# Optimization experiments

Measured on AMD Instinct MI355X. Metric: run time of the kernel, lower is better.

## Reference

```python
import jax, jax.numpy as jnp
import numpy as np

N, E = 50000, 800000
NFEAT, NHID, NCLASS = 128, 64, 40
NLAYERS = 4
DT, ALPHA, GAMMA = 1.0, 1.0, 1.0


def setup_inputs() -> dict:
    key = jax.random.key(0)
    ks = jax.random.split(key, 12)
    s = 1.0 / np.sqrt(NHID)
    inp = {
        'x': jax.random.normal(ks[0], (N, NFEAT), jnp.float32),
        'edge_index': jax.random.randint(ks[1], (2, E), 0, N, jnp.int64),
        # params stored as [in, out] matrices (torch Linear weight transposed)
        'enc_W': jax.random.uniform(ks[2], (NFEAT, NHID), jnp.float32, -s, s),
        'enc_b': jnp.zeros((NHID,), jnp.float32),
        'conv_W': jax.random.uniform(ks[3], (NHID, NHID), jnp.float32, -s, s),
        'conv_b': jnp.zeros((NHID,), jnp.float32),
        'res_W': jax.random.uniform(ks[4], (NHID, NHID), jnp.float32, -s, s),
        'res_b': jnp.zeros((NHID,), jnp.float32),
        'weight_mlp': jax.random.uniform(ks[5], (NHID, NHID), jnp.float32, -s, s),
        'lamda1': jnp.float32(1.0),
        'dec_W': jax.random.uniform(ks[6], (NHID, NCLASS), jnp.float32, -s, s),
        'dec_b': jnp.zeros((NCLASS,), jnp.float32),
    }
    return inp


def reference(x, edge_index, enc_W, enc_b, conv_W, conv_b, res_W, res_b,
              weight_mlp, lamda1, dec_W, dec_b):
    src, dst = edge_index[0], edge_index[1]
    # GCN symmetric normalization with self-loops (PyG GCNConv default)
    deg = jax.ops.segment_sum(jnp.ones((E,), x.dtype), dst, num_segments=N) + 1.0
    dinv = jax.lax.rsqrt(deg)                      # [N]
    enorm = (dinv[src] * dinv[dst])[:, None]       # [E,1]
    self_norm = (dinv * dinv)[:, None]             # [N,1]

    Y = jax.nn.relu(x @ enc_W + enc_b)             # [N,H]
    X = Y
    for _ in range(NLAYERS):
        Xs, Xd = X[src], X[dst]                    # [E,H] gathers
        x_new = jax.nn.relu((Xs - Xd) @ weight_mlp) * Xd
        ax3 = jax.ops.segment_sum(x_new, dst, num_segments=N)  # [N,H]
        # GCNConv: normalized aggregation of X@W plus self-loop, then bias
        xw = X @ conv_W
        conv = (jax.ops.segment_sum(xw[src] * enorm, dst, num_segments=N)
                + xw * self_norm + conv_b)
        # residual v1: -res(conv.lin(X)) = -(X@W_conv @ W_res + b_res)
        res = -(xw @ res_W + res_b)
        Y = Y + DT * (jax.nn.relu(conv + res) - ALPHA * Y - GAMMA * X)
        X = X + DT * (Y + lamda1 * ax3)
    return X @ dec_W + dec_b
```

## Files before the change

### kernel.cpp

```cpp
#include <hip/hip_runtime.h>

constexpr int H   = 64;
constexpr int NF  = 128;
constexpr int NC  = 40;
constexpr int CAP = 96;

typedef __attribute__((ext_vector_type(8))) short short8;
typedef __attribute__((ext_vector_type(4))) float f32x4;

constexpr int FRAG_ENC = 1536;
constexpr int FRAG_DEC = 3584;
constexpr int FRAG_TOT = 4352;

__device__ __forceinline__ unsigned int f2bf(float f) {
  unsigned int u = __float_as_uint(f);
  return (u + 0x7fffu + ((u >> 16) & 1u)) >> 16;
}
__device__ __forceinline__ float bf_lo(unsigned int v) { return __uint_as_float(v << 16); }
__device__ __forceinline__ float bf_hi(unsigned int v) { return __uint_as_float(v & 0xffff0000u); }
__device__ __forceinline__ short8 ld_frag(const uint4* frag, int idx) {
  uint4 u = frag[idx];
  short8 r; __builtin_memcpy(&r, &u, 16); return r;
}

__global__ void k_wcr(const float* __restrict__ Wconv, const float* __restrict__ resW,
                      float* __restrict__ Wcr) {
  int idx = blockIdx.x * 256 + threadIdx.x;
  int k = idx >> 6, n = idx & 63;
  float s = 0.0f;
  for (int j = 0; j < 64; ++j) s = fmaf(Wconv[k * 64 + j], resW[j * 64 + n], s);
  Wcr[idx] = s;
}

__global__ void k_prep(const float* __restrict__ Wmlp, const float* __restrict__ Wconv,
                       const float* __restrict__ Wcr, const float* __restrict__ encW,
                       const float* __restrict__ decW, uint4* __restrict__ frag) {
  int it = blockIdx.x * 256 + threadIdx.x;
  if (it >= FRAG_TOT) return;
  unsigned int h[8];
  if (it < FRAG_ENC) {
    int lane = it & 63;
    int kb = (it >> 6) & 1;
    int nb = (it >> 7) & 3;
    int w  = (it >> 9);
    int col = nb * 16 + (lane & 15);
    int k0 = kb * 32 + (lane >> 4) * 8;
    for (int i = 0; i < 8; ++i) {
      float v;
      if (w == 2)      v = Wcr[(k0 + i) * 64 + col];
      else if (w == 1) v = Wconv[(k0 + i) * 64 + col];
      else             v = Wmlp[(k0 + i) * 64 + col];
      h[i] = f2bf(v);
    }
  } else if (it < FRAG_DEC) {
    int e = it - FRAG_ENC;
    int lane = e & 63;
    int kb = (e >> 6) & 3;
    int nb = (e >> 8) & 3;
    int hh = (e >> 10);
    int col = nb * 16 + (lane & 15);
    int k0 = kb * 32 + (lane >> 4) * 8;
    for (int i = 0; i < 8; ++i) {
      float v = encW[(k0 + i) * H + col];
      unsigned int hb = f2bf(v);
      h[i] = (hh == 0) ? hb : f2bf(v - __uint_as_float(hb << 16));
    }
  } else {
    int e = it - FRAG_DEC;
    int lane = e & 63;
    int kb = (e >> 6) & 1;
    int hn = e >> 7;
    int nb = hn % 3, hh = hn / 3;
    int col = nb * 16 + (lane & 15);
    int k0 = kb * 32 + (lane >> 4) * 8;
    for (int i = 0; i < 8; ++i) {
      float v = (col < NC) ? decW[(k0 + i) * NC + col] : 0.0f;
      unsigned int hb = f2bf(v);
      h[i] = (hh == 0) ? hb : f2bf(v - __uint_as_float(hb << 16));
    }
  }
  uint4 u; u.x = h[0] | (h[1] << 16); u.y = h[2] | (h[3] << 16);
  u.z = h[4] | (h[5] << 16); u.w = h[6] | (h[7] << 16);
  frag[it] = u;
}

__global__ void __launch_bounds__(256)
k_buildenc(const float* __restrict__ x, const uint4* __restrict__ frag,
           const float* __restrict__ encb, float* __restrict__ X,
           const int* __restrict__ src, const int* __restrict__ dst,
           int* __restrict__ counts, unsigned short* __restrict__ srcs,
           int N, int E) {
  int nchunks = (E + 1023) >> 10;
  if ((int)blockIdx.x < nchunks) {
    int base = (blockIdx.x << 10) + threadIdx.x;
    int d[4], s[4], slot[4];
#pragma unroll
    for (int j = 0; j < 4; ++j) {
      int e = base + j * 256;
      bool v = e < E;
      d[j] = v ? dst[e] : -1;
      s[j] = v ? src[e] : 0;
    }
#pragma unroll
    for (int j = 0; j < 4; ++j)
      slot[j] = (d[j] >= 0) ? atomicAdd(&counts[d[j]], 1) : CAP;
#pragma unroll
    for (int j = 0; j < 4; ++j)
      if (d[j] >= 0 && slot[j] < CAP) srcs[d[j] * CAP + slot[j]] = (unsigned short)s[j];
  }
  int lane = threadIdx.x & 63;
  int row = lane & 15, g = lane >> 4;
  int wv = (blockIdx.x * blockDim.x + threadIdx.x) >> 6;
  int nwv = (gridDim.x * blockDim.x) >> 6;
  float bias[4];
#pragma unroll
  for (int nb = 0; nb < 4; ++nb) bias[nb] = encb[nb * 16 + row];
  int nrb = (N + 15) >> 4;
  for (int rb = wv; rb < nrb; rb += nwv) {
    int n0 = rb << 4;
    int rload = n0 + row; if (rload > N - 1) rload = N - 1;
    const float* xp = x + (size_t)rload * NF + g * 8;
    f32x4 acc[4];
#pragma unroll
    for (int nb = 0; nb < 4; ++nb) acc[nb] = (f32x4){bias[nb], bias[nb], bias[nb], bias[nb]};
#pragma unroll
    for (int kb = 0; kb < 4; ++kb) {
      float4 a0 = *(const float4*)(xp + kb * 32);
      float4 a1 = *(const float4*)(xp + kb * 32 + 4);
      float xv[8] = {a0.x, a0.y, a0.z, a0.w, a1.x, a1.y, a1.z, a1.w};
      short8 Ahi, Alo;
#pragma unroll
      for (int i = 0; i < 8; ++i) {
        unsigned int hb = f2bf(xv[i]);
        Ahi[i] = (short)hb;
        Alo[i] = (short)f2bf(xv[i] - __uint_as_float(hb << 16));
      }
#pragma unroll
      for (int nb = 0; nb < 4; ++nb) {
        short8 Bh = ld_frag(frag, FRAG_ENC + ((0 * 4 + nb) * 4 + kb) * 64 + lane);
        short8 Bl = ld_frag(frag, FRAG_ENC + ((1 * 4 + nb) * 4 + kb) * 64 + lane);
        acc[nb] = __builtin_amdgcn_mfma_f32_16x16x32_bf16(Ahi, Bh, acc[nb], 0, 0, 0);
        acc[nb] = __builtin_amdgcn_mfma_f32_16x16x32_bf16(Alo, Bh, acc[nb], 0, 0, 0);
        acc[nb] = __builtin_amdgcn_mfma_f32_16x16x32_bf16(Ahi, Bl, acc[nb], 0, 0, 0);
      }
    }
#pragma unroll
    for (int nb = 0; nb < 4; ++nb) {
      int col = nb * 16 + row;
#pragma unroll
      for (int j = 0; j < 4; ++j) {
        int n = n0 + g * 4 + j;
        if (n < N) X[(size_t)n * H + col] = fmaxf(acc[nb][j], 0.0f);
      }
    }
  }
}

__global__ void __launch_bounds__(256, 2)
k_xform(const float* __restrict__ X, const uint4* __restrict__ frag,
        const float* __restrict__ resb, const int* __restrict__ counts,
        unsigned int* __restrict__ xmwq, unsigned short* __restrict__ rbuf, int N) {
  int lane = threadIdx.x & 63;
  int row = lane & 15, g = lane >> 4;
  int wv = (blockIdx.x * blockDim.x + threadIdx.x) >> 6;
  int nwv = (gridDim.x * blockDim.x) >> 6;

  short8 B[3][4][2];
#pragma unroll
  for (int w = 0; w < 3; ++w)
#pragma unroll
    for (int nb = 0; nb < 4; ++nb)
#pragma unroll
      for (int kb = 0; kb < 2; ++kb)
        B[w][nb][kb] = ld_frag(frag, ((w * 4 + nb) * 2 + kb) * 64 + lane);
  float rbias[4];
#pragma unroll
  for (int nb = 0; nb < 4; ++nb) rbias[nb] = resb[nb * 16 + row];

  int nrb = (N + 15) >> 4;
  for (int rb = wv; rb < nrb; rb += nwv) {
    int n0 = rb << 4;
    int rload = n0 + row; if (rload > N - 1) rload = N - 1;
    const float* xp = X + (size_t)rload * H + g * 8;
    float xv[2][8];
    {
      float4 a0 = *(const float4*)(xp);
      float4 a1 = *(const float4*)(xp + 4);
      float4 b0 = *(const float4*)(xp + 32);
      float4 b1 = *(const float4*)(xp + 36);
      xv[0][0]=a0.x; xv[0][1]=a0.y; xv[0][2]=a0.z; xv[0][3]=a0.w;
      xv[0][4]=a1.x; xv[0][5]=a1.y; xv[0][6]=a1.z; xv[0][7]=a1.w;
      xv[1][0]=b0.x; xv[1][1]=b0.y; xv[1][2]=b0.z; xv[1][3]=b0.w;
      xv[1][4]=b1.x; xv[1][5]=b1.y; xv[1][6]=b1.z; xv[1][7]=b1.w;
    }
    short8 Ahi[2], Alo[2];
#pragma unroll
    for (int kb = 0; kb < 2; ++kb)
#pragma unroll
      for (int i = 0; i < 8; ++i) {
        float v = xv[kb][i];
        unsigned int hb = f2bf(v);
        Ahi[kb][i] = (short)hb;
        Alo[kb][i] = (short)f2bf(v - __uint_as_float(hb << 16));
      }
    f32x4 am[4], ac[4], ar[4];
#pragma unroll
    for (int nb = 0; nb < 4; ++nb) {
      am[nb] = (f32x4){0.f, 0.f, 0.f, 0.f};
      ac[nb] = (f32x4){0.f, 0.f, 0.f, 0.f};
      ar[nb] = (f32x4){rbias[nb], rbias[nb], rbias[nb], rbias[nb]};
    }
#pragma unroll
    for (int nb = 0; nb < 4; ++nb)
#pragma unroll
      for (int kb = 0; kb < 2; ++kb) {
        am[nb] = __builtin_amdgcn_mfma_f32_16x16x32_bf16(Ahi[kb], B[0][nb][kb], am[nb], 0, 0, 0);
        am[nb] = __builtin_amdgcn_mfma_f32_16x16x32_bf16(Alo[kb], B[0][nb][kb], am[nb], 0, 0, 0);
        ac[nb] = __builtin_amdgcn_mfma_f32_16x16x32_bf16(Ahi[kb], B[1][nb][kb], ac[nb], 0, 0, 0);
        ac[nb] = __builtin_amdgcn_mfma_f32_16x16x32_bf16(Alo[kb], B[1][nb][kb], ac[nb], 0, 0, 0);
        ar[nb] = __builtin_amdgcn_mfma_f32_16x16x32_bf16(Ahi[kb], B[2][nb][kb], ar[nb], 0, 0, 0);
        ar[nb] = __builtin_amdgcn_mfma_f32_16x16x32_bf16(Alo[kb], B[2][nb][kb], ar[nb], 0, 0, 0);
      }
    float dn4[4];
#pragma unroll
    for (int j = 0; j < 4; ++j) {
      int n = n0 + g * 4 + j; if (n > N - 1) n = N - 1;
      dn4[j] = rsqrtf((float)counts[n] + 1.0f);
    }
#pragma unroll
    for (int nb = 0; nb < 4; ++nb) {
      int col = nb * 16 + row;
#pragma unroll
      for (int j = 0; j < 4; ++j) {
        int n = n0 + g * 4 + j;
        if (n < N) {
          xmwq[(size_t)n * H + col] = f2bf(am[nb][j]) | (f2bf(ac[nb][j] * dn4[j]) << 16);
          rbuf[(size_t)n * H + col] = (unsigned short)f2bf(ar[nb][j]);
        }
      }
    }
  }
}

template<int DOX>
__global__ void __launch_bounds__(256)
k_updx(const unsigned int* __restrict__ xmwq_in, const unsigned short* __restrict__ rbuf_in,
       const unsigned short* __restrict__ srcs, const int* __restrict__ counts,
       const float* __restrict__ convb, const float* __restrict__ lam1,
       float* __restrict__ X, const uint4* __restrict__ frag,
       const float* __restrict__ resb,
       unsigned int* __restrict__ xmwq_out, unsigned short* __restrict__ rbuf_out, int N) {
  __shared__ float sX[16][68];
  int lane = threadIdx.x & 63;
  int w = threadIdx.x >> 6;
  int row = lane & 15, gg = lane >> 4;
  float cb = convb[lane];
  float lam = lam1[0];
  short8 Bw[3][2];
  float rbias = 0.0f;
  if (DOX) {
#pragma unroll
    for (int m = 0; m < 3; ++m)
#pragma unroll
      for (int kb = 0; kb < 2; ++kb)
        Bw[m][kb] = ld_frag(frag, ((m * 4 + w) * 2 + kb) * 64 + lane);
    rbias = resb[w * 16 + row];
  }
  int g = blockIdx.x;
  {
#pragma unroll
    for (int j = 0; j < 4; ++j) {
      int nig = w * 4 + j;
      int n = g * 16 + nig;
      bool act = n < N;
      int nn = act ? n : N - 1;
      size_t rowo = (size_t)nn * H + lane;
      unsigned int own = xmwq_in[rowo];
      float xmd = bf_lo(own), xwsd = bf_hi(own);
      float r = __uint_as_float((unsigned int)rbuf_in[rowo] << 16);
      float Xd = X[rowo];
      int cntfull = counts[nn];
      float dn = rsqrtf((float)cntfull + 1.0f);
      int cnt = cntfull < CAP ? cntfull : CAP;
      int sv0 = (lane < cnt) ? (int)srcs[nn * CAP + lane] : 0;
      int sv1 = (64 + lane < cnt) ? (int)srcs[nn * CAP + 64 + lane] : 0;
      float acc3 = 0.0f, accC = 0.0f;
      for (int e = 0; e < cnt; e += 16) {
        unsigned int v[16]; float m[16];
#pragma unroll
        for (int q = 0; q < 16; ++q) {
          int eq = e + q;
          bool valid = eq < cnt;
          int s = valid ? ((eq < 64) ? __builtin_amdgcn_readlane(sv0, eq)
                                     : __builtin_amdgcn_readlane(sv1, eq - 64))
                        : 0;
          v[q] = xmwq_in[(size_t)s * H + lane];
          m[q] = valid ? 1.0f : 0.0f;
        }
#pragma unroll
        for (int q = 0; q < 16; ++q) {
          acc3 += m[q] * fmaxf(bf_lo(v[q]) - xmd, 0.0f);
          accC += m[q] * bf_hi(v[q]);
        }
      }
      float conv = fmaf(dn, accC + xwsd, cb);
      float R = fmaxf(conv - r, 0.0f);
      float Xnew = R + lam * (acc3 * Xd);
      if (act) X[rowo] = Xnew;
      if (DOX) sX[nig][lane] = act ? Xnew : 0.0f;
    }
    if (DOX) {
      __syncthreads();
      short8 Ahi[2], Alo[2];
#pragma unroll
      for (int kb = 0; kb < 2; ++kb) {
        float4 a0 = *(const float4*)&sX[row][kb * 32 + gg * 8];
        float4 a1 = *(const float4*)&sX[row][kb * 32 + gg * 8 + 4];
        float xv[8] = {a0.x, a0.y, a0.z, a0.w, a1.x, a1.y, a1.z, a1.w};
#pragma unroll
        for (int i = 0; i < 8; ++i) {
          unsigned int hb = f2bf(xv[i]);
          Ahi[kb][i] = (short)hb;
          Alo[kb][i] = (short)f2bf(xv[i] - __uint_as_float(hb << 16));
        }
      }
      f32x4 am = (f32x4){0.f, 0.f, 0.f, 0.f};
      f32x4 ac = (f32x4){0.f, 0.f, 0.f, 0.f};
      f32x4 ar = (f32x4){rbias, rbias, rbias, rbias};
#pragma unroll
      for (int kb = 0; kb < 2; ++kb) {
        am = __builtin_amdgcn_mfma_f32_16x16x32_bf16(Ahi[kb], Bw[0][kb], am, 0, 0, 0);
        am = __builtin_amdgcn_mfma_f32_16x16x32_bf16(Alo[kb], Bw[0][kb], am, 0, 0, 0);
        ac = __builtin_amdgcn_mfma_f32_16x16x32_bf16(Ahi[kb], Bw[1][kb], ac, 0, 0, 0);
        ac = __builtin_amdgcn_mfma_f32_16x16x32_bf16(Alo[kb], Bw[1][kb], ac, 0, 0, 0);
        ar = __builtin_amdgcn_mfma_f32_16x16x32_bf16(Ahi[kb], Bw[2][kb], ar, 0, 0, 0);
        ar = __builtin_amdgcn_mfma_f32_16x16x32_bf16(Alo[kb], Bw[2][kb], ar, 0, 0, 0);
      }
      int col = w * 16 + row;
#pragma unroll
      for (int j = 0; j < 4; ++j) {
        int n = g * 16 + gg * 4 + j;
        if (n < N) {
          float dnn = rsqrtf((float)counts[n] + 1.0f);
          xmwq_out[(size_t)n * H + col] = f2bf(am[j]) | (f2bf(ac[j] * dnn) << 16);
          rbuf_out[(size_t)n * H + col] = (unsigned short)f2bf(ar[j]);
        }
      }
    }
  }
}

__global__ void __launch_bounds__(256)
k_dec(const float* __restrict__ X, const uint4* __restrict__ frag,
      const float* __restrict__ decb, float* __restrict__ out, int N) {
  int lane = threadIdx.x & 63;
  int row = lane & 15, g = lane >> 4;
  int wv = (blockIdx.x * blockDim.x + threadIdx.x) >> 6;
  int nwv = (gridDim.x * blockDim.x) >> 6;
  float bias[3];
#pragma unroll
  for (int nb = 0; nb < 3; ++nb) {
    int col = nb * 16 + row;
    bias[nb] = (col < NC) ? decb[col] : 0.0f;
  }
  int nrb = (N + 15) >> 4;
  for (int rb = wv; rb < nrb; rb += nwv) {
    int n0 = rb << 4;
    int rload = n0 + row; if (rload > N - 1) rload = N - 1;
    const float* xp = X + (size_t)rload * H + g * 8;
    f32x4 acc[3];
#pragma unroll
    for (int nb = 0; nb < 3; ++nb) acc[nb] = (f32x4){bias[nb], bias[nb], bias[nb], bias[nb]};
#pragma unroll
    for (int kb = 0; kb < 2; ++kb) {
      float4 a0 = *(const float4*)(xp + kb * 32);
      float4 a1 = *(const float4*)(xp + kb * 32 + 4);
      float xv[8] = {a0.x, a0.y, a0.z, a0.w, a1.x, a1.y, a1.z, a1.w};
      short8 Ahi, Alo;
#pragma unroll
      for (int i = 0; i < 8; ++i) {
        unsigned int hb = f2bf(xv[i]);
        Ahi[i] = (short)hb;
        Alo[i] = (short)f2bf(xv[i] - __uint_as_float(hb << 16));
      }
#pragma unroll
      for (int nb = 0; nb < 3; ++nb) {
        short8 Bh = ld_frag(frag, FRAG_DEC + ((0 * 3 + nb) * 2 + kb) * 64 + lane);
        short8 Bl = ld_frag(frag, FRAG_DEC + ((1 * 3 + nb) * 2 + kb) * 64 + lane);
        acc[nb] = __builtin_amdgcn_mfma_f32_16x16x32_bf16(Ahi, Bh, acc[nb], 0, 0, 0);
        acc[nb] = __builtin_amdgcn_mfma_f32_16x16x32_bf16(Alo, Bh, acc[nb], 0, 0, 0);
        acc[nb] = __builtin_amdgcn_mfma_f32_16x16x32_bf16(Ahi, Bl, acc[nb], 0, 0, 0);
      }
    }
#pragma unroll
    for (int nb = 0; nb < 3; ++nb) {
      int col = nb * 16 + row;
      if (col < NC) {
#pragma unroll
        for (int j = 0; j < 4; ++j) {
          int n = n0 + g * 4 + j;
          if (n < N) out[(size_t)n * NC + col] = acc[nb][j];
        }
      }
    }
  }
}

extern "C" void kernel_launch(void* const* d_in, const int* in_sizes, int n_in,
                              void* d_out, int out_size, void* d_ws, size_t ws_size,
                              hipStream_t stream) {
  const float* x    = (const float*)d_in[0];
  const int*   ei   = (const int*)d_in[1];
  const float* encW = (const float*)d_in[2];
  const float* encb = (const float*)d_in[3];
  const float* convW= (const float*)d_in[4];
  const float* convb= (const float*)d_in[5];
  const float* resW = (const float*)d_in[6];
  const float* resb = (const float*)d_in[7];
  const float* wmlp = (const float*)d_in[8];
  const float* lam1 = (const float*)d_in[9];
  const float* decW = (const float*)d_in[10];
  const float* decb = (const float*)d_in[11];
  int N = in_sizes[0] / NF;
  int E = in_sizes[1] / 2;
  const int* src = ei;
  const int* dst = ei + E;

  char* ws = (char*)d_ws;
  size_t off = 0;
  auto alloc = [&](size_t bytes) -> void* {
    void* p = ws + off;
    off = (off + bytes + 255) & ~(size_t)255;
    return p;
  };
  int*            counts = (int*)alloc((size_t)N * 4);
  unsigned short* srcs   = (unsigned short*)alloc((size_t)N * CAP * 2);
  float*          X      = (float*)alloc((size_t)N * H * 4);
  unsigned int*   xmwqA  = (unsigned int*)alloc((size_t)N * H * 4);
  unsigned int*   xmwqB  = (unsigned int*)alloc((size_t)N * H * 4);
  unsigned short* rbufA  = (unsigned short*)alloc((size_t)N * H * 2);
  unsigned short* rbufB  = (unsigned short*)alloc((size_t)N * H * 2);
  uint4*          frag   = (uint4*)alloc((size_t)FRAG_TOT * 16);
  float*          Wcr    = (float*)alloc(64 * 64 * 4);

  hipMemsetAsync(counts, 0, (size_t)N * 4, stream);

  const int tb = 256;
  k_wcr<<<16, tb, 0, stream>>>(convW, resW, Wcr);
  k_prep<<<(FRAG_TOT + tb - 1) / tb, tb, 0, stream>>>(wmlp, convW, Wcr, encW, decW, frag);
  k_buildenc<<<2048, tb, 0, stream>>>(x, frag, encb, X, src, dst, counts, srcs, N, E);
  k_xform<<<784, tb, 0, stream>>>(X, frag, resb, counts, xmwqA, rbufA, N);
  int ngrp = (N + 15) >> 4;
  k_updx<1><<<ngrp, tb, 0, stream>>>(xmwqA, rbufA, srcs, counts, convb, lam1, X,
                                     frag, resb, xmwqB, rbufB, N);
  k_updx<1><<<ngrp, tb, 0, stream>>>(xmwqB, rbufB, srcs, counts, convb, lam1, X,
                                     frag, resb, xmwqA, rbufA, N);
  k_updx<1><<<ngrp, tb, 0, stream>>>(xmwqA, rbufA, srcs, counts, convb, lam1, X,
                                     frag, resb, xmwqB, rbufB, N);
  k_updx<0><<<ngrp, tb, 0, stream>>>(xmwqB, rbufB, srcs, counts, convb, lam1, X,
                                     frag, resb, xmwqA, rbufA, N);
  k_dec<<<784, tb, 0, stream>>>(X, frag, decb, (float*)d_out, N);
}
```

Before: 269.3 us.

## Fuse first transform into encoder and decoder into last layer; precompute dinv

Folds the first-layer projection (xmwq/rbuf) into the encoder kernel through a shared-memory tile, so X is not re-read and one launch disappears. The decoder matmul moves into the last update kernel, and degree normalization is precomputed into a dinv array by a small kernel. Because counts are not final inside the fused encoder, the first update kernel applies the source-side dinv per gathered edge instead (SIN variant). This adds one extra dinv load per edge in layer one and removes the separate k_xform and k_dec passes over X.

After: 252.3 us. 1.07x faster.

```diff
diff --git a/kernel.cpp b/kernel.cpp
--- a/kernel.cpp
+++ b/kernel.cpp
@@ -30,6 +30,11 @@
   float s = 0.0f;
   for (int j = 0; j < 64; ++j) s = fmaf(Wconv[k * 64 + j], resW[j * 64 + n], s);
   Wcr[idx] = s;
+}
+
+__global__ void k_dinv(const int* __restrict__ counts, float* __restrict__ dinv, int N) {
+  int n = blockIdx.x * 256 + threadIdx.x;
+  if (n < N) dinv[n] = rsqrtf((float)counts[n] + 1.0f);
 }
 
 __global__ void k_prep(const float* __restrict__ Wmlp, const float* __restrict__ Wconv,
@@ -86,10 +91,13 @@
 
 __global__ void __launch_bounds__(256)
 k_buildenc(const float* __restrict__ x, const uint4* __restrict__ frag,
-           const float* __restrict__ encb, float* __restrict__ X,
+           const float* __restrict__ encb, const float* __restrict__ resb,
+           float* __restrict__ X,
+           unsigned int* __restrict__ xmwq, unsigned short* __restrict__ rbuf,
            const int* __restrict__ src, const int* __restrict__ dst,
            int* __restrict__ counts, unsigned short* __restrict__ srcs,
            int N, int E) {
+  __shared__ float sX[4][16][68];
   int nchunks = (E + 1023) >> 10;
   if ((int)blockIdx.x < nchunks) {
     int base = (blockIdx.x << 10) + threadIdx.x;
@@ -109,12 +117,16 @@
       if (d[j] >= 0 && slot[j] < CAP) srcs[d[j] * CAP + slot[j]] = (unsigned short)s[j];
   }
   int lane = threadIdx.x & 63;
+  int w = threadIdx.x >> 6;
   int row = lane & 15, g = lane >> 4;
   int wv = (blockIdx.x * blockDim.x + threadIdx.x) >> 6;
   int nwv = (gridDim.x * blockDim.x) >> 6;
   float bias[4];
 #pragma unroll
   for (int nb = 0; nb < 4; ++nb) bias[nb] = encb[nb * 16 + row];
+  float rbias[4];
+#pragma unroll
+  for (int nb = 0; nb < 4; ++nb) rbias[nb] = resb[nb * 16 + row];
   int nrb = (N + 15) >> 4;
   for (int rb = wv; rb < nrb; rb += nwv) {
     int n0 = rb << 4;
@@ -150,59 +162,24 @@
 #pragma unroll
       for (int j = 0; j < 4; ++j) {
         int n = n0 + g * 4 + j;
-        if (n < N) X[(size_t)n * H + col] = fmaxf(acc[nb][j], 0.0f);
-      }
-    }
-  }
-}
-
-__global__ void __launch_bounds__(256, 2)
-k_xform(const float* __restrict__ X, const uint4* __restrict__ frag,
-        const float* __restrict__ resb, const int* __restrict__ counts,
-        unsigned int* __restrict__ xmwq, unsigned short* __restrict__ rbuf, int N) {
-  int lane = threadIdx.x & 63;
-  int row = lane & 15, g = lane >> 4;
-  int wv = (blockIdx.x * blockDim.x + threadIdx.x) >> 6;
-  int nwv = (gridDim.x * blockDim.x) >> 6;
-
-  short8 B[3][4][2];
-#pragma unroll
-  for (int w = 0; w < 3; ++w)
-#pragma unroll
-    for (int nb = 0; nb < 4; ++nb)
-#pragma unroll
-      for (int kb = 0; kb < 2; ++kb)
-        B[w][nb][kb] = ld_frag(frag, ((w * 4 + nb) * 2 + kb) * 64 + lane);
-  float rbias[4];
-#pragma unroll
-  for (int nb = 0; nb < 4; ++nb) rbias[nb] = resb[nb * 16 + row];
-
-  int nrb = (N + 15) >> 4;
-  for (int rb = wv; rb < nrb; rb += nwv) {
-    int n0 = rb << 4;
-    int rload = n0 + row; if (rload > N - 1) rload = N - 1;
-    const float* xp = X + (size_t)rload * H + g * 8;
-    float xv[2][8];
-    {
-      float4 a0 = *(const float4*)(xp);
-      float4 a1 = *(const float4*)(xp + 4);
-      float4 b0 = *(const float4*)(xp + 32);
-      float4 b1 = *(const float4*)(xp + 36);
-      xv[0][0]=a0.x; xv[0][1]=a0.y; xv[0][2]=a0.z; xv[0][3]=a0.w;
-      xv[0][4]=a1.x; xv[0][5]=a1.y; xv[0][6]=a1.z; xv[0][7]=a1.w;
-      xv[1][0]=b0.x; xv[1][1]=b0.y; xv[1][2]=b0.z; xv[1][3]=b0.w;
-      xv[1][4]=b1.x; xv[1][5]=b1.y; xv[1][6]=b1.z; xv[1][7]=b1.w;
+        float val = fmaxf(acc[nb][j], 0.0f);
+        if (n < N) X[(size_t)n * H + col] = val;
+        sX[w][g * 4 + j][col] = (n < N) ? val : 0.0f;
+      }
     }
     short8 Ahi[2], Alo[2];
 #pragma unroll
-    for (int kb = 0; kb < 2; ++kb)
+    for (int kb = 0; kb < 2; ++kb) {
+      float4 a0 = *(const float4*)&sX[w][row][kb * 32 + g * 8];
+      float4 a1 = *(const float4*)&sX[w][row][kb * 32 + g * 8 + 4];
+      float xv[8] = {a0.x, a0.y, a0.z, a0.w, a1.x, a1.y, a1.z, a1.w};
 #pragma unroll
       for (int i = 0; i < 8; ++i) {
-        float v = xv[kb][i];
-        unsigned int hb = f2bf(v);
+        unsigned int hb = f2bf(xv[i]);
         Ahi[kb][i] = (short)hb;
-        Alo[kb][i] = (short)f2bf(v - __uint_as_float(hb << 16));
-      }
+        Alo[kb][i] = (short)f2bf(xv[i] - __uint_as_float(hb << 16));
+      }
+    }
     f32x4 am[4], ac[4], ar[4];
 #pragma unroll
     for (int nb = 0; nb < 4; ++nb) {
@@ -214,19 +191,16 @@
     for (int nb = 0; nb < 4; ++nb)
 #pragma unroll
       for (int kb = 0; kb < 2; ++kb) {
-        am[nb] = __builtin_amdgcn_mfma_f32_16x16x32_bf16(Ahi[kb], B[0][nb][kb], am[nb], 0, 0, 0);
-        am[nb] = __builtin_amdgcn_mfma_f32_16x16x32_bf16(Alo[kb], B[0][nb][kb], am[nb], 0, 0, 0);
-        ac[nb] = __builtin_amdgcn_mfma_f32_16x16x32_bf16(Ahi[kb], B[1][nb][kb], ac[nb], 0, 0, 0);
-        ac[nb] = __builtin_amdgcn_mfma_f32_16x16x32_bf16(Alo[kb], B[1][nb][kb], ac[nb], 0, 0, 0);
-        ar[nb] = __builtin_amdgcn_mfma_f32_16x16x32_bf16(Ahi[kb], B[2][nb][kb], ar[nb], 0, 0, 0);
-        ar[nb] = __builtin_amdgcn_mfma_f32_16x16x32_bf16(Alo[kb], B[2][nb][kb], ar[nb], 0, 0, 0);
-      }
-    float dn4[4];
-#pragma unroll
-    for (int j = 0; j < 4; ++j) {
-      int n = n0 + g * 4 + j; if (n > N - 1) n = N - 1;
-      dn4[j] = rsqrtf((float)counts[n] + 1.0f);
-    }
+        short8 B0 = ld_frag(frag, ((0 * 4 + nb) * 2 + kb) * 64 + lane);
+        short8 B1 = ld_frag(frag, ((1 * 4 + nb) * 2 + kb) * 64 + lane);
+        short8 B2 = ld_frag(frag, ((2 * 4 + nb) * 2 + kb) * 64 + lane);
+        am[nb] = __builtin_amdgcn_mfma_f32_16x16x32_bf16(Ahi[kb], B0, am[nb], 0, 0, 0);
+        am[nb] = __builtin_amdgcn_mfma_f32_16x16x32_bf16(Alo[kb], B0, am[nb], 0, 0, 0);
+        ac[nb] = __builtin_amdgcn_mfma_f32_16x16x32_bf16(Ahi[kb], B1, ac[nb], 0, 0, 0);
+        ac[nb] = __builtin_amdgcn_mfma_f32_16x16x32_bf16(Alo[kb], B1, ac[nb], 0, 0, 0);
+        ar[nb] = __builtin_amdgcn_mfma_f32_16x16x32_bf16(Ahi[kb], B2, ar[nb], 0, 0, 0);
+        ar[nb] = __builtin_amdgcn_mfma_f32_16x16x32_bf16(Alo[kb], B2, ar[nb], 0, 0, 0);
+      }
 #pragma unroll
     for (int nb = 0; nb < 4; ++nb) {
       int col = nb * 16 + row;
@@ -234,7 +208,7 @@
       for (int j = 0; j < 4; ++j) {
         int n = n0 + g * 4 + j;
         if (n < N) {
-          xmwq[(size_t)n * H + col] = f2bf(am[nb][j]) | (f2bf(ac[nb][j] * dn4[j]) << 16);
+          xmwq[(size_t)n * H + col] = f2bf(am[nb][j]) | (f2bf(ac[nb][j]) << 16);
           rbuf[(size_t)n * H + col] = (unsigned short)f2bf(ar[nb][j]);
         }
       }
@@ -242,75 +216,118 @@
   }
 }
 
-template<int DOX>
+template<int DOX, int SIN, int DODEC>
 __global__ void __launch_bounds__(256)
 k_updx(const unsigned int* __restrict__ xmwq_in, const unsigned short* __restrict__ rbuf_in,
        const unsigned short* __restrict__ srcs, const int* __restrict__ counts,
+       const float* __restrict__ dinv,
        const float* __restrict__ convb, const float* __restrict__ lam1,
        float* __restrict__ X, const uint4* __restrict__ frag,
-       const float* __restrict__ resb,
-       unsigned int* __restrict__ xmwq_out, unsigned short* __restrict__ rbuf_out, int N) {
+       const float* __restrict__ resb, const float* __restrict__ decb,
+       unsigned int* __restrict__ xmwq_out, unsigned short* __restrict__ rbuf_out,
+       float* __restrict__ out, int N) {
   __shared__ float sX[16][68];
   int lane = threadIdx.x & 63;
   int w = threadIdx.x >> 6;
   int row = lane & 15, gg = lane >> 4;
   float cb = convb[lane];
   float lam = lam1[0];
-  short8 Bw[3][2];
-  float rbias = 0.0f;
+  int g = blockIdx.x;
+#pragma unroll
+  for (int j = 0; j < 4; ++j) {
+    int nig = w * 4 + j;
+    int n = g * 16 + nig;
+    bool act = n < N;
+    int nn = act ? n : N - 1;
+    size_t rowo = (size_t)nn * H + lane;
+    unsigned int own = xmwq_in[rowo];
+    float dn = dinv[nn];
+    float xmd = bf_lo(own);
+    float xwsd = SIN ? bf_hi(own) * dn : bf_hi(own);
+    float r = __uint_as_float((unsigned int)rbuf_in[rowo] << 16);
+    float Xd = X[rowo];
+    int cntfull = counts[nn];
+    int cnt = cntfull < CAP ? cntfull : CAP;
+    int sv0 = (lane < cnt) ? (int)srcs[nn * CAP + lane] : 0;
+    int sv1 = (64 + lane < cnt) ? (int)srcs[nn * CAP + 64 + lane] : 0;
+    float acc3 = 0.0f, accC = 0.0f;
+    for (int e = 0; e < cnt; e += 16) {
+      unsigned int v[16]; float m[16]; float ds[16];
+#pragma unroll
+      for (int q = 0; q < 16; ++q) {
+        int eq = e + q;
+        bool valid = eq < cnt;
+        int s = valid ? ((eq < 64) ? __builtin_amdgcn_readlane(sv0, eq)
+                                   : __builtin_amdgcn_readlane(sv1, eq - 64))
+                      : 0;
+        v[q] = xmwq_in[(size_t)s * H + lane];
+        if (SIN) ds[q] = dinv[s];
+        m[q] = valid ? 1.0f : 0.0f;
+      }
+#pragma unroll
+      for (int q = 0; q < 16; ++q) {
+        acc3 += m[q] * fmaxf(bf_lo(v[q]) - xmd, 0.0f);
+        float t = bf_hi(v[q]);
+        if (SIN) t *= ds[q];
+        accC += m[q] * t;
+      }
+    }
+    float conv = fmaf(dn, accC + xwsd, cb);
+    float R = fmaxf(conv - r, 0.0f);
+    float Xnew = R + lam * (acc3 * Xd);
+    if (!DODEC) { if (act) X[rowo] = Xnew; }
+    if (DOX || DODEC) sX[nig][lane] = act ? Xnew : 0.0f;
+  }
   if (DOX) {
+    __syncthreads();
+    short8 Bw[3][2];
 #pragma unroll
     for (int m = 0; m < 3; ++m)
 #pragma unroll
       for (int kb = 0; kb < 2; ++kb)
         Bw[m][kb] = ld_frag(frag, ((m * 4 + w) * 2 + kb) * 64 + lane);
-    rbias = resb[w * 16 + row];
-  }
-  int g = blockIdx.x;
-  {
+    float rbias = resb[w * 16 + row];
+    short8 Ahi[2], Alo[2];
+#pragma unroll
+    for (int kb = 0; kb < 2; ++kb) {
+      float4 a0 = *(const float4*)&sX[row][kb * 32 + gg * 8];
+      float4 a1 = *(const float4*)&sX[row][kb * 32 + gg * 8 + 4];
+      float xv[8] = {a0.x, a0.y, a0.z, a0.w, a1.x, a1.y, a1.z, a1.w};
+#pragma unroll
+      for (int i = 0; i < 8; ++i) {
+        unsigned int hb = f2bf(xv[i]);
+        Ahi[kb][i] = (short)hb;
+        Alo[kb][i] = (short)f2bf(xv[i] - __uint_as_float(hb << 16));
+      }
+    }
+    f32x4 am = (f32x4){0.f, 0.f, 0.f, 0.f};
+    f32x4 ac = (f32x4){0.f, 0.f, 0.f, 0.f};
+    f32x4 ar = (f32x4){rbias, rbias, rbias, rbias};
+#pragma unroll
+    for (int kb = 0; kb < 2; ++kb) {
+      am = __builtin_amdgcn_mfma_f32_16x16x32_bf16(Ahi[kb], Bw[0][kb], am, 0, 0, 0);
+      am = __builtin_amdgcn_mfma_f32_16x16x32_bf16(Alo[kb], Bw[0][kb], am, 0, 0, 0);
+      ac = __builtin_amdgcn_mfma_f32_16x16x32_bf16(Ahi[kb], Bw[1][kb], ac, 0, 0, 0);
+      ac = __builtin_amdgcn_mfma_f32_16x16x32_bf16(Alo[kb], Bw[1][kb], ac, 0, 0, 0);
+      ar = __builtin_amdgcn_mfma_f32_16x16x32_bf16(Ahi[kb], Bw[2][kb], ar, 0, 0, 0);
+      ar = __builtin_amdgcn_mfma_f32_16x16x32_bf16(Alo[kb], Bw[2][kb], ar, 0, 0, 0);
+    }
+    int col = w * 16 + row;
 #pragma unroll
     for (int j = 0; j < 4; ++j) {
-      int nig = w * 4 + j;
-      int n = g * 16 + nig;
-      bool act = n < N;
-      int nn = act ? n : N - 1;
-      size_t rowo = (size_t)nn * H + lane;
-      unsigned int own = xmwq_in[rowo];
-      float xmd = bf_lo(own), xwsd = bf_hi(own);
-      float r = __uint_as_float((unsigned int)rbuf_in[rowo] << 16);
-      float Xd = X[rowo];
-      int cntfull = counts[nn];
-      float dn = rsqrtf((float)cntfull + 1.0f);
-      int cnt = cntfull < CAP ? cntfull : CAP;
-      int sv0 = (lane < cnt) ? (int)srcs[nn * CAP + lane] : 0;
-      int sv1 = (64 + lane < cnt) ? (int)srcs[nn * CAP + 64 + lane] : 0;
-      float acc3 = 0.0f, accC = 0.0f;
-      for (int e = 0; e < cnt; e += 16) {
-        unsigned int v[16]; float m[16];
-#pragma unroll
-        for (int q = 0; q < 16; ++q) {
-          int eq = e + q;
-          bool valid = eq < cnt;
-          int s = valid ? ((eq < 64) ? __builtin_amdgcn_readlane(sv0, eq)
-                                     : __builtin_amdgcn_readlane(sv1, eq - 64))
-                        : 0;
-          v[q] = xmwq_in[(size_t)s * H + lane];
-          m[q] = valid ? 1.0f : 0.0f;
-        }
-#pragma unroll
-        for (int q = 0; q < 16; ++q) {
-          acc3 += m[q] * fmaxf(bf_lo(v[q]) - xmd, 0.0f);
-          accC += m[q] * bf_hi(v[q]);
-        }
-      }
-      float conv = fmaf(dn, accC + xwsd, cb);
-      float R = fmaxf(conv - r, 0.0f);
-      float Xnew = R + lam * (acc3 * Xd);
-      if (act) X[rowo] = Xnew;
-      if (DOX) sX[nig][lane] = act ? Xnew : 0.0f;
-    }
-    if (DOX) {
-      __syncthreads();
+      int n = g * 16 + gg * 4 + j;
+      if (n < N) {
+        float dnn = dinv[n];
+        xmwq_out[(size_t)n * H + col] = f2bf(am[j]) | (f2bf(ac[j] * dnn) << 16);
+        rbuf_out[(size_t)n * H + col] = (unsigned short)f2bf(ar[j]);
+      }
+    }
+  }
+  if (DODEC) {
+    __syncthreads();
+    if (w < 3) {
+      int col = w * 16 + row;
+      float bias = (col < NC) ? decb[col] : 0.0f;
       short8 Ahi[2], Alo[2];
 #pragma unroll
       for (int kb = 0; kb < 2; ++kb) {
@@ -324,82 +341,20 @@
           Alo[kb][i] = (short)f2bf(xv[i] - __uint_as_float(hb << 16));
         }
       }
-      f32x4 am = (f32x4){0.f, 0.f, 0.f, 0.f};
-      f32x4 ac = (f32x4){0.f, 0.f, 0.f, 0.f};
-      f32x4 ar = (f32x4){rbias, rbias, rbias, rbias};
+      f32x4 acc = (f32x4){bias, bias, bias, bias};
 #pragma unroll
       for (int kb = 0; kb < 2; ++kb) {
-        am = __builtin_amdgcn_mfma_f32_16x16x32_bf16(Ahi[kb], Bw[0][kb], am, 0, 0, 0);
-        am = __builtin_amdgcn_mfma_f32_16x16x32_bf16(Alo[kb], Bw[0][kb], am, 0, 0, 0);
-        ac = __builtin_amdgcn_mfma_f32_16x16x32_bf16(Ahi[kb], Bw[1][kb], ac, 0, 0, 0);
-        ac = __builtin_amdgcn_mfma_f32_16x16x32_bf16(Alo[kb], Bw[1][kb], ac, 0, 0, 0);
-        ar = __builtin_amdgcn_mfma_f32_16x16x32_bf16(Ahi[kb], Bw[2][kb], ar, 0, 0, 0);
-        ar = __builtin_amdgcn_mfma_f32_16x16x32_bf16(Alo[kb], Bw[2][kb], ar, 0, 0, 0);
-      }
-      int col = w * 16 + row;
-#pragma unroll
-      for (int j = 0; j < 4; ++j) {
-        int n = g * 16 + gg * 4 + j;
-        if (n < N) {
-          float dnn = rsqrtf((float)counts[n] + 1.0f);
-          xmwq_out[(size_t)n * H + col] = f2bf(am[j]) | (f2bf(ac[j] * dnn) << 16);
-          rbuf_out[(size_t)n * H + col] = (unsigned short)f2bf(ar[j]);
-        }
-      }
-    }
-  }
-}
-
-__global__ void __launch_bounds__(256)
-k_dec(const float* __restrict__ X, const uint4* __restrict__ frag,
-      const float* __restrict__ decb, float* __restrict__ out, int N) {
-  int lane = threadIdx.x & 63;
-  int row = lane & 15, g = lane >> 4;
-  int wv = (blockIdx.x * blockDim.x + threadIdx.x) >> 6;
-  int nwv = (gridDim.x * blockDim.x) >> 6;
-  float bias[3];
-#pragma unroll
-  for (int nb = 0; nb < 3; ++nb) {
-    int col = nb * 16 + row;
-    bias[nb] = (col < NC) ? decb[col] : 0.0f;
-  }
-  int nrb = (N + 15) >> 4;
-  for (int rb = wv; rb < nrb; rb += nwv) {
-    int n0 = rb << 4;
-    int rload = n0 + row; if (rload > N - 1) rload = N - 1;
-    const float* xp = X + (size_t)rload * H + g * 8;
-    f32x4 acc[3];
-#pragma unroll
-    for (int nb = 0; nb < 3; ++nb) acc[nb] = (f32x4){bias[nb], bias[nb], bias[nb], bias[nb]};
-#pragma unroll
-    for (int kb = 0; kb < 2; ++kb) {
-      float4 a0 = *(const float4*)(xp + kb * 32);
-      float4 a1 = *(const float4*)(xp + kb * 32 + 4);
-      float xv[8] = {a0.x, a0.y, a0.z, a0.w, a1.x, a1.y, a1.z, a1.w};
-      short8 Ahi, Alo;
-#pragma unroll
-      for (int i = 0; i < 8; ++i) {
-        unsigned int hb = f2bf(xv[i]);
-        Ahi[i] = (short)hb;
-        Alo[i] = (short)f2bf(xv[i] - __uint_as_float(hb << 16));
-      }
-#pragma unroll
-      for (int nb = 0; nb < 3; ++nb) {
-        short8 Bh = ld_frag(frag, FRAG_DEC + ((0 * 3 + nb) * 2 + kb) * 64 + lane);
-        short8 Bl = ld_frag(frag, FRAG_DEC + ((1 * 3 + nb) * 2 + kb) * 64 + lane);
-        acc[nb] = __builtin_amdgcn_mfma_f32_16x16x32_bf16(Ahi, Bh, acc[nb], 0, 0, 0);
-        acc[nb] = __builtin_amdgcn_mfma_f32_16x16x32_bf16(Alo, Bh, acc[nb], 0, 0, 0);
-        acc[nb] = __builtin_amdgcn_mfma_f32_16x16x32_bf16(Ahi, Bl, acc[nb], 0, 0, 0);
-      }
-    }
-#pragma unroll
-    for (int nb = 0; nb < 3; ++nb) {
-      int col = nb * 16 + row;
+        short8 Bh = ld_frag(frag, FRAG_DEC + ((0 * 3 + w) * 2 + kb) * 64 + lane);
+        short8 Bl = ld_frag(frag, FRAG_DEC + ((1 * 3 + w) * 2 + kb) * 64 + lane);
+        acc = __builtin_amdgcn_mfma_f32_16x16x32_bf16(Ahi[kb], Bh, acc, 0, 0, 0);
+        acc = __builtin_amdgcn_mfma_f32_16x16x32_bf16(Alo[kb], Bh, acc, 0, 0, 0);
+        acc = __builtin_amdgcn_mfma_f32_16x16x32_bf16(Ahi[kb], Bl, acc, 0, 0, 0);
+      }
       if (col < NC) {
 #pragma unroll
         for (int j = 0; j < 4; ++j) {
-          int n = n0 + g * 4 + j;
-          if (n < N) out[(size_t)n * NC + col] = acc[nb][j];
+          int n = g * 16 + gg * 4 + j;
+          if (n < N) out[(size_t)n * NC + col] = acc[j];
         }
       }
     }
@@ -436,6 +391,7 @@
   int*            counts = (int*)alloc((size_t)N * 4);
   unsigned short* srcs   = (unsigned short*)alloc((size_t)N * CAP * 2);
   float*          X      = (float*)alloc((size_t)N * H * 4);
+  float*          dinv   = (float*)alloc((size_t)N * 4);
   unsigned int*   xmwqA  = (unsigned int*)alloc((size_t)N * H * 4);
   unsigned int*   xmwqB  = (unsigned int*)alloc((size_t)N * H * 4);
   unsigned short* rbufA  = (unsigned short*)alloc((size_t)N * H * 2);
@@ -448,16 +404,17 @@
   const int tb = 256;
   k_wcr<<<16, tb, 0, stream>>>(convW, resW, Wcr);
   k_prep<<<(FRAG_TOT + tb - 1) / tb, tb, 0, stream>>>(wmlp, convW, Wcr, encW, decW, frag);
-  k_buildenc<<<2048, tb, 0, stream>>>(x, frag, encb, X, src, dst, counts, srcs, N, E);
-  k_xform<<<784, tb, 0, stream>>>(X, frag, resb, counts, xmwqA, rbufA, N);
+  k_buildenc<<<2048, tb, 0, stream>>>(x, frag, encb, resb, X, xmwqA, rbufA,
+                                      src, dst, counts, srcs, N, E);
+  k_dinv<<<(N + tb - 1) / tb, tb, 0, stream>>>(counts, dinv, N);
   int ngrp = (N + 15) >> 4;
-  k_updx<1><<<ngrp, tb, 0, stream>>>(xmwqA, rbufA, srcs, counts, convb, lam1, X,
-                                     frag, resb, xmwqB, rbufB, N);
-  k_updx<1><<<ngrp, tb, 0, stream>>>(xmwqB, rbufB, srcs, counts, convb, lam1, X,
-                                     frag, resb, xmwqA, rbufA, N);
-  k_updx<1><<<ngrp, tb, 0, stream>>>(xmwqA, rbufA, srcs, counts, convb, lam1, X,
-                                     frag, resb, xmwqB, rbufB, N);
-  k_updx<0><<<ngrp, tb, 0, stream>>>(xmwqB, rbufB, srcs, counts, convb, lam1, X,
-                                     frag, resb, xmwqA, rbufA, N);
-  k_dec<<<784, tb, 0, stream>>>(X, frag, decb, (float*)d_out, N);
-}
+  float* outp = (float*)d_out;
+  k_updx<1,1,0><<<ngrp, tb, 0, stream>>>(xmwqA, rbufA, srcs, counts, dinv, convb, lam1, X,
+                                         frag, resb, decb, xmwqB, rbufB, outp, N);
+  k_updx<1,0,0><<<ngrp, tb, 0, stream>>>(xmwqB, rbufB, srcs, counts, dinv, convb, lam1, X,
+                                         frag, resb, decb, xmwqA, rbufA, outp, N);
+  k_updx<1,0,0><<<ngrp, tb, 0, stream>>>(xmwqA, rbufA, srcs, counts, dinv, convb, lam1, X,
+                                         frag, resb, decb, xmwqB, rbufB, outp, N);
+  k_updx<0,0,1><<<ngrp, tb, 0, stream>>>(xmwqB, rbufB, srcs, counts, dinv, convb, lam1, X,
+                                         frag, resb, decb, xmwqA, rbufA, outp, N);
+}
```
